# Performance work log

Hardware: AMD Instinct MI355X
Metric: run time of the kernel (lower is better)

Reference implementation:

```python
import jax, jax.numpy as jnp
import numpy as np

PATCH_LEN = 16
PATCH_STRIDE = 8
DIM = 512
NUM_HEADS = 8
HEAD_DIM = DIM // NUM_HEADS
NUM_LAYERS = 4
MLP_HIDDEN = 4 * DIM
ROPE_BASE = 10000.0
LN_EPS = 1e-5


def setup_inputs() -> dict:
    key = jax.random.key(0)
    ks = jax.random.split(key, 20)
    B, T, C = 4, 8192, 7
    s = 0.02
    inp = {
        "x": jax.random.normal(ks[0], (B, T, C), dtype=jnp.float32),
        "W_emb": jax.random.normal(ks[1], (PATCH_LEN * C, DIM), dtype=jnp.float32) * s,
        "b_emb": jnp.zeros((DIM,), jnp.float32),
        "ln1_g": jnp.ones((NUM_LAYERS, DIM), jnp.float32),
        "ln1_b": jnp.zeros((NUM_LAYERS, DIM), jnp.float32),
        "W_qkv": jax.random.normal(ks[2], (NUM_LAYERS, DIM, 3 * DIM), dtype=jnp.float32) * s,
        "b_qkv": jnp.zeros((NUM_LAYERS, 3 * DIM), jnp.float32),
        "W_proj": jax.random.normal(ks[3], (NUM_LAYERS, DIM, DIM), dtype=jnp.float32) * s,
        "b_proj": jnp.zeros((NUM_LAYERS, DIM), jnp.float32),
        "ln2_g": jnp.ones((NUM_LAYERS, DIM), jnp.float32),
        "ln2_b": jnp.zeros((NUM_LAYERS, DIM), jnp.float32),
        "W_mlp1": jax.random.normal(ks[4], (NUM_LAYERS, DIM, MLP_HIDDEN), dtype=jnp.float32) * s,
        "b_mlp1": jnp.zeros((NUM_LAYERS, MLP_HIDDEN), jnp.float32),
        "W_mlp2": jax.random.normal(ks[5], (NUM_LAYERS, MLP_HIDDEN, DIM), dtype=jnp.float32) * s,
        "b_mlp2": jnp.zeros((NUM_LAYERS, DIM), jnp.float32),
        "lnf_g": jnp.ones((DIM,), jnp.float32),
        "lnf_b": jnp.zeros((DIM,), jnp.float32),
    }
    return inp


def _layer_norm(x, g, b):
    mu = jnp.mean(x, axis=-1, keepdims=True)
    var = jnp.mean(jnp.square(x - mu), axis=-1, keepdims=True)
    return (x - mu) * jax.lax.rsqrt(var + LN_EPS) * g + b


def _rotate_half(x):
    x1, x2 = jnp.split(x, 2, axis=-1)
    return jnp.concatenate((-x2, x1), axis=-1)


def _rope_cos_sin(seq_len):
    t = jnp.arange(seq_len, dtype=jnp.float32)
    inv_freq = 1.0 / (ROPE_BASE ** (jnp.arange(0, HEAD_DIM, 2, dtype=jnp.float32) / HEAD_DIM))
    freqs = jnp.outer(t, inv_freq)                      # [L, hd/2]
    emb = jnp.concatenate((freqs, freqs), axis=-1)      # [L, hd]
    return jnp.cos(emb), jnp.sin(emb)


def _forward(x, W_emb, b_emb, ln1_g, ln1_b, W_qkv, b_qkv, W_proj, b_proj,
             ln2_g, ln2_b, W_mlp1, b_mlp1, W_mlp2, b_mlp2, lnf_g, lnf_b):
    B, T, C = x.shape
    n = (T - PATCH_LEN) // PATCH_STRIDE + 1
    # torch unfold: [B, n, C, patch_len], then flattened as (C, patch_len)
    idx = jnp.arange(n)[:, None] * PATCH_STRIDE + jnp.arange(PATCH_LEN)[None, :]  # [n, P]
    patches = x[:, idx, :]                              # [B, n, P, C]
    patches = patches.transpose(0, 1, 3, 2).reshape(B, n, C * PATCH_LEN)
    emb = patches @ W_emb + b_emb                       # [B, n, D]

    cos, sin = _rope_cos_sin(n)                         # [n, hd]
    cos = cos[None, None, :, :]
    sin = sin[None, None, :, :]
    scale = HEAD_DIM ** -0.5

    h = emb
    for i in range(NUM_LAYERS):
        # --- attention ---
        y = _layer_norm(h, ln1_g[i], ln1_b[i])
        qkv = (y @ W_qkv[i] + b_qkv[i]).reshape(B, n, 3, NUM_HEADS, HEAD_DIM)
        qkv = qkv.transpose(2, 0, 3, 1, 4)              # [3, B, H, n, hd]
        q, k, v = qkv[0], qkv[1], qkv[2]
        q = q * cos + _rotate_half(q) * sin
        k = k * cos + _rotate_half(k) * sin
        attn = jax.nn.softmax(jnp.einsum('bhqd,bhkd->bhqk', q, k) * scale, axis=-1)
        o = jnp.einsum('bhqk,bhkd->bhqd', attn, v)      # [B, H, n, hd]
        o = o.transpose(0, 2, 1, 3).reshape(B, n, DIM)
        h = h + (o @ W_proj[i] + b_proj[i])
        # --- mlp ---
        y = _layer_norm(h, ln2_g[i], ln2_b[i])
        y = jax.nn.gelu(y @ W_mlp1[i] + b_mlp1[i], approximate=False)
        h = h + (y @ W_mlp2[i] + b_mlp2[i])

    x_out = _layer_norm(h, lnf_g, lnf_b)
    return emb, x_out


def reference(x, W_emb, b_emb, ln1_g, ln1_b, W_qkv, b_qkv, W_proj, b_proj,
              ln2_g, ln2_b, W_mlp1, b_mlp1, W_mlp2, b_mlp2, lnf_g, lnf_b):
    return _forward(x, W_emb, b_emb, ln1_g, ln1_b, W_qkv, b_qkv, W_proj, b_proj,
                    ln2_g, ln2_b, W_mlp1, b_mlp1, W_mlp2, b_mlp2, lnf_g, lnf_b)
```

## Files before the change

### kernel.cpp

```cpp
#include <hip/hip_runtime.h>
#include <hip/hip_bf16.h>
#include <math.h>

#define B_SZ 4
#define T_LEN 8192
#define C_IN 7
#define NPATCH 1023
#define DIM 512
#define NH 8
#define HD 64
#define NLAYERS 4
#define MLP_HID 2048
#define M_ROWS (B_SZ * NPATCH)
#define KEMB 128
#define LN_EPS 1e-5f

typedef __attribute__((ext_vector_type(8))) short short8;
typedef __attribute__((ext_vector_type(4))) float float4v;

static __device__ __forceinline__ unsigned short f2bf(float f) {
  __hip_bfloat16 h = __float2bfloat16(f);
  return *reinterpret_cast<unsigned short*>(&h);
}
static __device__ __forceinline__ float bf2f(unsigned short u) {
  return __uint_as_float(((unsigned)u) << 16);
}

__global__ __launch_bounds__(256) void patch_kernel(
    const float* __restrict__ x, unsigned short* __restrict__ Pm) {
  int idx = blockIdx.x * 256 + threadIdx.x;
  if (idx >= M_ROWS * KEMB) return;
  int row = idx >> 7, c = idx & 127;
  float v = 0.f;
  if (c < 112) {
    int b = row / NPATCH, i = row - b * NPATCH;
    int ci = c >> 4, p = c & 15;
    v = x[((size_t)b * T_LEN + (size_t)i * 8 + p) * C_IN + ci];
  }
  Pm[idx] = f2bf(v);
}

__global__ __launch_bounds__(256) void wemb_cvt_kernel(
    const float* __restrict__ W, unsigned short* __restrict__ Wt) {
  int idx = blockIdx.x * 256 + threadIdx.x;
  if (idx >= DIM * KEMB) return;
  int n = idx >> 7, k = idx & 127;
  float v = (k < 112) ? W[(size_t)k * DIM + n] : 0.f;
  Wt[idx] = f2bf(v);
}

template <bool BF>
__global__ __launch_bounds__(256) void ln_kernel(
    const float* __restrict__ in, const float* __restrict__ g,
    const float* __restrict__ bb, void* __restrict__ outv, int M) {
  int row = blockIdx.x * 4 + (threadIdx.x >> 6);
  if (row >= M) return;
  int lane = threadIdx.x & 63;
  const float* xr = in + (size_t)row * DIM;
  float v[8];
  float s = 0.f;
  #pragma unroll
  for (int k = 0; k < 8; ++k) { v[k] = xr[lane + 64 * k]; s += v[k]; }
  #pragma unroll
  for (int off = 32; off; off >>= 1) s += __shfl_down(s, off);
  s = __shfl(s, 0);
  float mu = s * (1.f / DIM);
  float q = 0.f;
  #pragma unroll
  for (int k = 0; k < 8; ++k) { float d = v[k] - mu; q = fmaf(d, d, q); }
  #pragma unroll
  for (int off = 32; off; off >>= 1) q += __shfl_down(q, off);
  q = __shfl(q, 0);
  float rstd = rsqrtf(q * (1.f / DIM) + LN_EPS);
  #pragma unroll
  for (int k = 0; k < 8; ++k) {
    int d = lane + 64 * k;
    float r = (v[k] - mu) * rstd * g[d] + bb[d];
    if (BF)
      ((unsigned short*)outv)[(size_t)row * DIM + d] = f2bf(r);
    else
      ((float*)outv)[(size_t)row * DIM + d] = r;
  }
}

__global__ __launch_bounds__(256) void wcvt_kernel(
    const float* __restrict__ W, unsigned short* __restrict__ Wt, int K, int N) {
  __shared__ float tile[32][33];
  int n0 = blockIdx.x * 32, k0 = blockIdx.y * 32, L = blockIdx.z;
  const float* Ws = W + (size_t)L * K * N;
  unsigned short* Wd = Wt + (size_t)L * K * N;
  int tx = threadIdx.x & 31, ty = threadIdx.x >> 5;
  #pragma unroll
  for (int i = 0; i < 4; ++i)
    tile[ty + i * 8][tx] = Ws[(size_t)(k0 + ty + i * 8) * N + n0 + tx];
  __syncthreads();
  #pragma unroll
  for (int i = 0; i < 4; ++i)
    Wd[(size_t)(n0 + ty + i * 8) * K + k0 + tx] = f2bf(tile[tx][ty + i * 8]);
}

__global__ __launch_bounds__(256) void rope_tab_kernel(float2* __restrict__ tab) {
  int idx = blockIdx.x * 256 + threadIdx.x;
  if (idx >= NPATCH * 32) return;
  int i = idx >> 5, j = idx & 31;
  float inv = powf(10000.0f, -(float)j * (1.0f / 32.0f));
  float sn, cs;
  sincosf((float)i * inv, &sn, &cs);
  tab[idx] = make_float2(cs, sn);
}

template <int TM, int TN, int EPI>
__global__ __launch_bounds__(256) void mfma_gemm(
    const unsigned short* __restrict__ A, const unsigned short* __restrict__ Bt,
    const float* __restrict__ bias, const float* __restrict__ res,
    float* __restrict__ Cf, float* __restrict__ Cf2,
    unsigned short* __restrict__ Cb, const float2* __restrict__ rtab,
    int M, int N, int K) {
  constexpr int WM = TM / 2, WN = TN / 2;
  constexpr int NI = WM / 16, NJ = WN / 16;
  constexpr int ACH = TM * 4;
  constexpr int TCH = (TM + TN) * 4;
  constexpr int CH = TCH / 256;
  __shared__ __align__(16) unsigned short As[2][TM][40];
  __shared__ __align__(16) unsigned short Bs[2][TN][40];
  const int bm = blockIdx.y * TM;
  const int bn = blockIdx.x * TN;
  const int tid = threadIdx.x;
  const int lane = tid & 63, wave = tid >> 6;
  const int quad = lane >> 4, l16 = lane & 15;
  const int wm = (wave & 1) * WM;
  const int wn = (wave >> 1) * WN;

  float4v acc[NI][NJ];
  #pragma unroll
  for (int i = 0; i < NI; ++i)
    #pragma unroll
    for (int j = 0; j < NJ; ++j)
      acc[i][j] = (float4v){0.f, 0.f, 0.f, 0.f};

  uint4 pr[CH];
  auto load_regs = [&](int kk) {
    #pragma unroll
    for (int it = 0; it < CH; ++it) {
      int c = tid + it * 256;
      if (c < ACH) {
        int row = c >> 2, ch = (c & 3) * 8;
        int gm = bm + row;
        pr[it] = make_uint4(0u, 0u, 0u, 0u);
        if (gm < M) pr[it] = *(const uint4*)(A + (size_t)gm * K + kk + ch);
      } else {
        int c2 = c - ACH;
        int row = c2 >> 2, ch = (c2 & 3) * 8;
        pr[it] = *(const uint4*)(Bt + (size_t)(bn + row) * K + kk + ch);
      }
    }
  };

  load_regs(0);
  int buf = 0;
  for (int k0 = 0; k0 < K; k0 += 32, buf ^= 1) {
    #pragma unroll
    for (int it = 0; it < CH; ++it) {
      int c = tid + it * 256;
      if (c < ACH)
        *(uint4*)&As[buf][c >> 2][(c & 3) * 8] = pr[it];
      else {
        int c2 = c - ACH;
        *(uint4*)&Bs[buf][c2 >> 2][(c2 & 3) * 8] = pr[it];
      }
    }
    if (k0 + 32 < K) load_regs(k0 + 32);
    __syncthreads();
    short8 af[NI], bfr[NJ];
    #pragma unroll
    for (int i = 0; i < NI; ++i)
      af[i] = *(const short8*)&As[buf][wm + i * 16 + l16][quad * 8];
    #pragma unroll
    for (int j = 0; j < NJ; ++j)
      bfr[j] = *(const short8*)&Bs[buf][wn + j * 16 + l16][quad * 8];
    #pragma unroll
    for (int i = 0; i < NI; ++i)
      #pragma unroll
      for (int j = 0; j < NJ; ++j)
        acc[i][j] = __builtin_amdgcn_mfma_f32_16x16x32_bf16(
            af[i], bfr[j], acc[i][j], 0, 0, 0);
  }

  if (EPI == 6) {
    const int sec = (bn + wn) >> 9;
    #pragma unroll
    for (int i = 0; i < NI; ++i) {
      int gm0 = bm + wm + i * 16 + quad * 4;
      #pragma unroll
      for (int r = 0; r < 4; ++r) {
        int gm = gm0 + r;
        if (gm >= M) continue;
        size_t rowoff = (size_t)gm * N;
        if (sec < 2) {
          int ip = gm; if (ip >= 2046) ip -= 2046; if (ip >= 1023) ip -= 1023;
          float sc = (sec == 0) ? 0.125f : 1.f;
          #pragma unroll
          for (int j = 0; j < 2; ++j) {
            int gn = bn + wn + j * 16 + l16;
            float v0 = acc[i][j][r] + bias[gn];
            float v1 = acc[i][j + 2][r] + bias[gn + 32];
            float2 t = rtab[ip * 32 + j * 16 + l16];
            Cb[rowoff + gn]      = f2bf((v0 * t.x - v1 * t.y) * sc);
            Cb[rowoff + gn + 32] = f2bf((v1 * t.x + v0 * t.y) * sc);
          }
        } else {
          #pragma unroll
          for (int j = 0; j < 4; ++j) {
            int gn = bn + wn + j * 16 + l16;
            Cb[rowoff + gn] = f2bf(acc[i][j][r] + bias[gn]);
          }
        }
      }
    }
    return;
  }

  #pragma unroll
  for (int j = 0; j < NJ; ++j) {
    int gn = bn + wn + j * 16 + l16;
    float bv = bias[gn];
    #pragma unroll
    for (int i = 0; i < NI; ++i) {
      int gm0 = bm + wm + i * 16 + quad * 4;
      #pragma unroll
      for (int r = 0; r < 4; ++r) {
        int gm = gm0 + r;
        if (gm < M) {
          float v = acc[i][j][r] + bv;
          size_t off = (size_t)gm * N + gn;
          if (EPI == 1) {
            Cf[off] = v + res[off];
          } else if (EPI == 2) {
            Cb[off] = f2bf(0.5f * v * (1.f + erff(v * 0.70710678118f)));
          } else if (EPI == 3) {
            Cb[off] = f2bf(v);
          } else {
            Cf[off] = v;
            Cf2[off] = v;
          }
        }
      }
    }
  }
}

#define APITCH 72

__global__ __launch_bounds__(256) void attn_kernel(
    const unsigned short* __restrict__ qkvb, unsigned short* __restrict__ o) {
  const int qt0 = blockIdx.x * 64;
  const int h = blockIdx.y;
  const int b = blockIdx.z;
  const int tid = threadIdx.x;
  const int lane = tid & 63, wave = tid >> 6;
  const int quad = lane >> 4, l16 = lane & 15;

  __shared__ __align__(16) unsigned short Qs[64][APITCH];
  __shared__ __align__(16) unsigned short Ks[64][APITCH];
  __shared__ __align__(16) unsigned short Vt[HD][APITCH];
  __shared__ __align__(16) unsigned short Ps[4][16][APITCH];

  const int sr = tid >> 2;
  const int sc0 = (tid & 3) * 16;

  {
    int qi = qt0 + sr;
    uint4 a = make_uint4(0u, 0u, 0u, 0u), b2 = a;
    if (qi < NPATCH) {
      const uint4* src = (const uint4*)(qkvb + (size_t)(b * NPATCH + qi) * (3 * DIM) + h * HD + sc0);
      a = src[0]; b2 = src[1];
    }
    *(uint4*)&Qs[sr][sc0] = a;
    *(uint4*)&Qs[sr][sc0 + 8] = b2;
  }

  uint4 pk0, pk1, pv0, pv1;
  auto load_kv = [&](int j0) {
    int j = j0 + sr;
    pk0 = pk1 = pv0 = pv1 = make_uint4(0u, 0u, 0u, 0u);
    if (j < NPATCH) {
      const unsigned short* baseb = qkvb + (size_t)(b * NPATCH + j) * (3 * DIM) + h * HD;
      pk0 = *(const uint4*)(baseb + DIM + sc0);
      pk1 = *(const uint4*)(baseb + DIM + sc0 + 8);
      pv0 = *(const uint4*)(baseb + 2 * DIM + sc0);
      pv1 = *(const uint4*)(baseb + 2 * DIM + sc0 + 8);
    }
  };
  load_kv(0);
  __syncthreads();

  short8 aq0 = *(const short8*)&Qs[wave * 16 + l16][quad * 8];
  short8 aq1 = *(const short8*)&Qs[wave * 16 + l16][32 + quad * 8];

  float4v accO[4];
  #pragma unroll
  for (int j2 = 0; j2 < 4; ++j2) accO[j2] = (float4v){0.f, 0.f, 0.f, 0.f};
  float m_run[4] = {-1e30f, -1e30f, -1e30f, -1e30f};
  float l_run[4] = {0.f, 0.f, 0.f, 0.f};

  for (int j0 = 0; j0 < NPATCH; j0 += 64) {
    {
      *(uint4*)&Ks[sr][sc0] = pk0;
      *(uint4*)&Ks[sr][sc0 + 8] = pk1;
      unsigned short vs[16];
      *(uint4*)&vs[0] = pv0;
      *(uint4*)&vs[8] = pv1;
      #pragma unroll
      for (int u = 0; u < 16; ++u) Vt[sc0 + u][sr] = vs[u];
    }
    __syncthreads();
    if (j0 + 64 < NPATCH) load_kv(j0 + 64);

    float4v s[4];
    #pragma unroll
    for (int j = 0; j < 4; ++j) {
      s[j] = (float4v){0.f, 0.f, 0.f, 0.f};
      short8 bk0 = *(const short8*)&Ks[j * 16 + l16][quad * 8];
      short8 bk1 = *(const short8*)&Ks[j * 16 + l16][32 + quad * 8];
      s[j] = __builtin_amdgcn_mfma_f32_16x16x32_bf16(aq0, bk0, s[j], 0, 0, 0);
      s[j] = __builtin_amdgcn_mfma_f32_16x16x32_bf16(aq1, bk1, s[j], 0, 0, 0);
    }

    float mx[4], al[4], ts[4];
    #pragma unroll
    for (int r = 0; r < 4; ++r)
      mx[r] = fmaxf(fmaxf(s[0][r], s[1][r]), fmaxf(s[2][r], s[3][r]));
    #pragma unroll
    for (int mask = 1; mask < 16; mask <<= 1)
      #pragma unroll
      for (int r = 0; r < 4; ++r)
        mx[r] = fmaxf(mx[r], __shfl_xor(mx[r], mask));
    #pragma unroll
    for (int r = 0; r < 4; ++r) {
      float mnew = fmaxf(m_run[r], mx[r]);
      al[r] = __expf(m_run[r] - mnew);
      m_run[r] = mnew;
      ts[r] = 0.f;
    }
    #pragma unroll
    for (int j = 0; j < 4; ++j) {
      bool valid = (j0 + j * 16 + l16) < NPATCH;
      #pragma unroll
      for (int r = 0; r < 4; ++r) {
        float p = valid ? __expf(s[j][r] - m_run[r]) : 0.f;
        ts[r] += p;
        Ps[wave][quad * 4 + r][j * 16 + l16] = f2bf(p);
      }
    }
    #pragma unroll
    for (int mask = 1; mask < 16; mask <<= 1)
      #pragma unroll
      for (int r = 0; r < 4; ++r)
        ts[r] += __shfl_xor(ts[r], mask);
    #pragma unroll
    for (int r = 0; r < 4; ++r) l_run[r] = l_run[r] * al[r] + ts[r];
    #pragma unroll
    for (int j2 = 0; j2 < 4; ++j2)
      #pragma unroll
      for (int r = 0; r < 4; ++r)
        accO[j2][r] *= al[r];

    short8 pa0 = *(const short8*)&Ps[wave][l16][quad * 8];
    short8 pa1 = *(const short8*)&Ps[wave][l16][32 + quad * 8];
    #pragma unroll
    for (int j2 = 0; j2 < 4; ++j2) {
      short8 v0 = *(const short8*)&Vt[j2 * 16 + l16][quad * 8];
      short8 v1 = *(const short8*)&Vt[j2 * 16 + l16][32 + quad * 8];
      accO[j2] = __builtin_amdgcn_mfma_f32_16x16x32_bf16(pa0, v0, accO[j2], 0, 0, 0);
      accO[j2] = __builtin_amdgcn_mfma_f32_16x16x32_bf16(pa1, v1, accO[j2], 0, 0, 0);
    }
    __syncthreads();
  }

  #pragma unroll
  for (int r = 0; r < 4; ++r) {
    int qi = qt0 + wave * 16 + quad * 4 + r;
    if (qi < NPATCH) {
      float inv = 1.f / l_run[r];
      size_t off = (size_t)(b * NPATCH + qi) * DIM + h * HD + l16;
      #pragma unroll
      for (int j2 = 0; j2 < 4; ++j2)
        o[off + j2 * 16] = f2bf(accO[j2][r] * inv);
    }
  }
}

extern "C" void kernel_launch(void* const* d_in, const int* in_sizes, int n_in,
                              void* d_out, int out_size, void* d_ws, size_t ws_size,
                              hipStream_t stream) {
  const float* x      = (const float*)d_in[0];
  const float* W_emb  = (const float*)d_in[1];
  const float* b_emb  = (const float*)d_in[2];
  const float* ln1_g  = (const float*)d_in[3];
  const float* ln1_b  = (const float*)d_in[4];
  const float* W_qkv  = (const float*)d_in[5];
  const float* b_qkv  = (const float*)d_in[6];
  const float* W_proj = (const float*)d_in[7];
  const float* b_proj = (const float*)d_in[8];
  const float* ln2_g  = (const float*)d_in[9];
  const float* ln2_b  = (const float*)d_in[10];
  const float* W_mlp1 = (const float*)d_in[11];
  const float* b_mlp1 = (const float*)d_in[12];
  const float* W_mlp2 = (const float*)d_in[13];
  const float* b_mlp2 = (const float*)d_in[14];
  const float* lnf_g  = (const float*)d_in[15];
  const float* lnf_b  = (const float*)d_in[16];
  float* out = (float*)d_out;

  float* h              = (float*)d_ws;
  unsigned short* qkvb  = (unsigned short*)(h + (size_t)M_ROWS * DIM);
  unsigned short* midbf = qkvb;
  unsigned short* ybf   = qkvb + (size_t)M_ROWS * MLP_HID;
  unsigned short* obf   = ybf;
  unsigned short* wqkv_t  = ybf + (size_t)M_ROWS * DIM;
  unsigned short* wproj_t = wqkv_t  + (size_t)NLAYERS * DIM * 3 * DIM;
  unsigned short* wmlp1_t = wproj_t + (size_t)NLAYERS * DIM * DIM;
  unsigned short* wmlp2_t = wmlp1_t + (size_t)NLAYERS * DIM * MLP_HID;
  float2* rtab = (float2*)(wmlp2_t + (size_t)NLAYERS * MLP_HID * DIM);
  unsigned short* Pm    = (unsigned short*)(rtab + (size_t)NPATCH * 32);
  unsigned short* Wembt = Pm + (size_t)M_ROWS * KEMB;

  wcvt_kernel<<<dim3(3 * DIM / 32, DIM / 32, NLAYERS), 256, 0, stream>>>(W_qkv,  wqkv_t,  DIM, 3 * DIM);
  wcvt_kernel<<<dim3(DIM / 32, DIM / 32, NLAYERS),     256, 0, stream>>>(W_proj, wproj_t, DIM, DIM);
  wcvt_kernel<<<dim3(MLP_HID / 32, DIM / 32, NLAYERS), 256, 0, stream>>>(W_mlp1, wmlp1_t, DIM, MLP_HID);
  wcvt_kernel<<<dim3(DIM / 32, MLP_HID / 32, NLAYERS), 256, 0, stream>>>(W_mlp2, wmlp2_t, MLP_HID, DIM);
  rope_tab_kernel<<<(NPATCH * 32 + 255) / 256, 256, 0, stream>>>(rtab);
  patch_kernel<<<(M_ROWS * KEMB + 255) / 256, 256, 0, stream>>>(x, Pm);
  wemb_cvt_kernel<<<(DIM * KEMB + 255) / 256, 256, 0, stream>>>(W_emb, Wembt);

  const int MT64 = (M_ROWS + 63) / 64;
  const int LNG = (M_ROWS + 3) / 4;

  mfma_gemm<64, 64, 5><<<dim3(DIM / 64, MT64), 256, 0, stream>>>(
      Pm, Wembt, b_emb, nullptr, out, h, nullptr, nullptr, M_ROWS, DIM, KEMB);

  for (int L = 0; L < NLAYERS; ++L) {
    ln_kernel<true><<<LNG, 256, 0, stream>>>(h, ln1_g + L * DIM, ln1_b + L * DIM, ybf, M_ROWS);
    mfma_gemm<64, 128, 6><<<dim3(3 * DIM / 128, MT64), 256, 0, stream>>>(
        ybf, wqkv_t + (size_t)L * DIM * 3 * DIM, b_qkv + L * 3 * DIM,
        nullptr, nullptr, nullptr, qkvb, rtab, M_ROWS, 3 * DIM, DIM);
    attn_kernel<<<dim3((NPATCH + 63) / 64, NH, B_SZ), 256, 0, stream>>>(qkvb, obf);
    mfma_gemm<64, 64, 1><<<dim3(DIM / 64, MT64), 256, 0, stream>>>(
        obf, wproj_t + (size_t)L * DIM * DIM, b_proj + L * DIM,
        h, h, nullptr, nullptr, nullptr, M_ROWS, DIM, DIM);
    ln_kernel<true><<<LNG, 256, 0, stream>>>(h, ln2_g + L * DIM, ln2_b + L * DIM, ybf, M_ROWS);
    mfma_gemm<64, 128, 2><<<dim3(MLP_HID / 128, MT64), 256, 0, stream>>>(
        ybf, wmlp1_t + (size_t)L * DIM * MLP_HID, b_mlp1 + L * MLP_HID,
        nullptr, nullptr, nullptr, midbf, nullptr, M_ROWS, MLP_HID, DIM);
    mfma_gemm<64, 64, 1><<<dim3(DIM / 64, MT64), 256, 0, stream>>>(
        midbf, wmlp2_t + (size_t)L * MLP_HID * DIM, b_mlp2 + L * DIM,
        h, h, nullptr, nullptr, nullptr, M_ROWS, DIM, MLP_HID);
  }

  ln_kernel<false><<<LNG, 256, 0, stream>>>(h, lnf_g, lnf_b, out + (size_t)M_ROWS * DIM, M_ROWS);
}
```

Baseline: 694.2 us.

## Restructure attention loop: K in registers, double-buffered V, lazy rescale

The attention kernel now loads K tiles straight from global memory into registers in MFMA operand layout, which removes the K shared-memory tile. V is transposed into a double-buffered shared tile using packed 32-bit writes, so the trailing barrier per iteration goes away. The online softmax skips rescaling unless some row's max grows by more than a threshold, and the row-sum reduction is deferred to the end. MFMA sections are wrapped in s_setprio. In exchange it uses more registers for the K prefetch, and the lazy rescale relies on exponent headroom staying bounded.

```diff
diff --git a/kernel.cpp b/kernel.cpp
--- a/kernel.cpp
+++ b/kernel.cpp
@@ -261,13 +261,11 @@
   const int quad = lane >> 4, l16 = lane & 15;
 
   __shared__ __align__(16) unsigned short Qs[64][APITCH];
-  __shared__ __align__(16) unsigned short Ks[64][APITCH];
-  __shared__ __align__(16) unsigned short Vt[HD][APITCH];
+  __shared__ __align__(16) unsigned short Vt[2][HD][APITCH];
   __shared__ __align__(16) unsigned short Ps[4][16][APITCH];
 
   const int sr = tid >> 2;
   const int sc0 = (tid & 3) * 16;
-
   {
     int qi = qt0 + sr;
     uint4 a = make_uint4(0u, 0u, 0u, 0u), b2 = a;
@@ -279,19 +277,34 @@
     *(uint4*)&Qs[sr][sc0 + 8] = b2;
   }
 
-  uint4 pk0, pk1, pv0, pv1;
-  auto load_kv = [&](int j0) {
-    int j = j0 + sr;
-    pk0 = pk1 = pv0 = pv1 = make_uint4(0u, 0u, 0u, 0u);
-    if (j < NPATCH) {
-      const unsigned short* baseb = qkvb + (size_t)(b * NPATCH + j) * (3 * DIM) + h * HD;
-      pk0 = *(const uint4*)(baseb + DIM + sc0);
-      pk1 = *(const uint4*)(baseb + DIM + sc0 + 8);
-      pv0 = *(const uint4*)(baseb + 2 * DIM + sc0);
-      pv1 = *(const uint4*)(baseb + 2 * DIM + sc0 + 8);
-    }
+  const int kp = tid & 31, dg = tid >> 5;
+  uint4 pv0, pv1;
+  auto load_v = [&](int j0) {
+    pv0 = pv1 = make_uint4(0u, 0u, 0u, 0u);
+    int j = j0 + 2 * kp;
+    const unsigned short* vb = qkvb + (size_t)(b * NPATCH + j) * (3 * DIM) + 2 * DIM + h * HD + dg * 8;
+    if (j < NPATCH)     pv0 = *(const uint4*)vb;
+    if (j + 1 < NPATCH) pv1 = *(const uint4*)(vb + 3 * DIM);
   };
-  load_kv(0);
+
+  const unsigned short* kbase = qkvb + (size_t)b * NPATCH * (3 * DIM) + DIM + (size_t)h * HD;
+  uint4 nk0[4], nk1[4];
+  auto load_k = [&](int j0) {
+    #pragma unroll
+    for (int j = 0; j < 4; ++j) {
+      int row = j0 + j * 16 + l16;
+      nk0[j] = make_uint4(0u, 0u, 0u, 0u);
+      nk1[j] = nk0[j];
+      if (row < NPATCH) {
+        const uint4* kr = (const uint4*)(kbase + (size_t)row * (3 * DIM) + quad * 8);
+        nk0[j] = kr[0];
+        nk1[j] = kr[4];
+      }
+    }
+  };
+
+  load_v(0);
+  load_k(0);
   __syncthreads();
 
   short8 aq0 = *(const short8*)&Qs[wave * 16 + l16][quad * 8];
@@ -301,32 +314,37 @@
   #pragma unroll
   for (int j2 = 0; j2 < 4; ++j2) accO[j2] = (float4v){0.f, 0.f, 0.f, 0.f};
   float m_run[4] = {-1e30f, -1e30f, -1e30f, -1e30f};
-  float l_run[4] = {0.f, 0.f, 0.f, 0.f};
-
-  for (int j0 = 0; j0 < NPATCH; j0 += 64) {
+  float lp[4] = {0.f, 0.f, 0.f, 0.f};
+
+  int buf = 0;
+  for (int j0 = 0; j0 < NPATCH; j0 += 64, buf ^= 1) {
     {
-      *(uint4*)&Ks[sr][sc0] = pk0;
-      *(uint4*)&Ks[sr][sc0 + 8] = pk1;
-      unsigned short vs[16];
-      *(uint4*)&vs[0] = pv0;
-      *(uint4*)&vs[8] = pv1;
-      #pragma unroll
-      for (int u = 0; u < 16; ++u) Vt[sc0 + u][sr] = vs[u];
+      unsigned short va[8], vb8[8];
+      *(uint4*)&va[0] = pv0;
+      *(uint4*)&vb8[0] = pv1;
+      #pragma unroll
+      for (int u = 0; u < 8; ++u) {
+        unsigned pk = (unsigned)va[u] | ((unsigned)vb8[u] << 16);
+        *(unsigned*)&Vt[buf][dg * 8 + u][2 * kp] = pk;
+      }
     }
     __syncthreads();
-    if (j0 + 64 < NPATCH) load_kv(j0 + 64);
 
     float4v s[4];
+    __builtin_amdgcn_s_setprio(1);
     #pragma unroll
     for (int j = 0; j < 4; ++j) {
       s[j] = (float4v){0.f, 0.f, 0.f, 0.f};
-      short8 bk0 = *(const short8*)&Ks[j * 16 + l16][quad * 8];
-      short8 bk1 = *(const short8*)&Ks[j * 16 + l16][32 + quad * 8];
-      s[j] = __builtin_amdgcn_mfma_f32_16x16x32_bf16(aq0, bk0, s[j], 0, 0, 0);
-      s[j] = __builtin_amdgcn_mfma_f32_16x16x32_bf16(aq1, bk1, s[j], 0, 0, 0);
-    }
-
-    float mx[4], al[4], ts[4];
+      s[j] = __builtin_amdgcn_mfma_f32_16x16x32_bf16(
+          aq0, __builtin_bit_cast(short8, nk0[j]), s[j], 0, 0, 0);
+      s[j] = __builtin_amdgcn_mfma_f32_16x16x32_bf16(
+          aq1, __builtin_bit_cast(short8, nk1[j]), s[j], 0, 0, 0);
+    }
+    __builtin_amdgcn_s_setprio(0);
+
+    if (j0 + 64 < NPATCH) { load_k(j0 + 64); load_v(j0 + 64); }
+
+    float mx[4];
     #pragma unroll
     for (int r = 0; r < 4; ++r)
       mx[r] = fmaxf(fmaxf(s[0][r], s[1][r]), fmaxf(s[2][r], s[3][r]));
@@ -335,12 +353,18 @@
       #pragma unroll
       for (int r = 0; r < 4; ++r)
         mx[r] = fmaxf(mx[r], __shfl_xor(mx[r], mask));
-    #pragma unroll
-    for (int r = 0; r < 4; ++r) {
-      float mnew = fmaxf(m_run[r], mx[r]);
-      al[r] = __expf(m_run[r] - mnew);
-      m_run[r] = mnew;
-      ts[r] = 0.f;
+    float g = fmaxf(fmaxf(mx[0] - m_run[0], mx[1] - m_run[1]),
+                    fmaxf(mx[2] - m_run[2], mx[3] - m_run[3]));
+    if (!__all(g <= 8.f)) {
+      #pragma unroll
+      for (int r = 0; r < 4; ++r) {
+        float mnew = fmaxf(m_run[r], mx[r]);
+        float al = __expf(m_run[r] - mnew);
+        m_run[r] = mnew;
+        lp[r] *= al;
+        #pragma unroll
+        for (int j2 = 0; j2 < 4; ++j2) accO[j2][r] *= al;
+      }
     }
     #pragma unroll
     for (int j = 0; j < 4; ++j) {
@@ -348,40 +372,35 @@
       #pragma unroll
       for (int r = 0; r < 4; ++r) {
         float p = valid ? __expf(s[j][r] - m_run[r]) : 0.f;
-        ts[r] += p;
+        lp[r] += p;
         Ps[wave][quad * 4 + r][j * 16 + l16] = f2bf(p);
       }
     }
-    #pragma unroll
-    for (int mask = 1; mask < 16; mask <<= 1)
-      #pragma unroll
-      for (int r = 0; r < 4; ++r)
-        ts[r] += __shfl_xor(ts[r], mask);
-    #pragma unroll
-    for (int r = 0; r < 4; ++r) l_run[r] = l_run[r] * al[r] + ts[r];
-    #pragma unroll
-    for (int j2 = 0; j2 < 4; ++j2)
-      #pragma unroll
-      for (int r = 0; r < 4; ++r)
-        accO[j2][r] *= al[r];
 
     short8 pa0 = *(const short8*)&Ps[wave][l16][quad * 8];
     short8 pa1 = *(const short8*)&Ps[wave][l16][32 + quad * 8];
+    __builtin_amdgcn_s_setprio(1);
     #pragma unroll
     for (int j2 = 0; j2 < 4; ++j2) {
-      short8 v0 = *(const short8*)&Vt[j2 * 16 + l16][quad * 8];
-      short8 v1 = *(const short8*)&Vt[j2 * 16 + l16][32 + quad * 8];
+      short8 v0 = *(const short8*)&Vt[buf][j2 * 16 + l16][quad * 8];
+      short8 v1 = *(const short8*)&Vt[buf][j2 * 16 + l16][32 + quad * 8];
       accO[j2] = __builtin_amdgcn_mfma_f32_16x16x32_bf16(pa0, v0, accO[j2], 0, 0, 0);
       accO[j2] = __builtin_amdgcn_mfma_f32_16x16x32_bf16(pa1, v1, accO[j2], 0, 0, 0);
     }
-    __syncthreads();
-  }
+    __builtin_amdgcn_s_setprio(0);
+  }
+
+  #pragma unroll
+  for (int mask = 1; mask < 16; mask <<= 1)
+    #pragma unroll
+    for (int r = 0; r < 4; ++r)
+      lp[r] += __shfl_xor(lp[r], mask);
 
   #pragma unroll
   for (int r = 0; r < 4; ++r) {
     int qi = qt0 + wave * 16 + quad * 4 + r;
     if (qi < NPATCH) {
-      float inv = 1.f / l_run[r];
+      float inv = 1.f / lp[r];
       size_t off = (size_t)(b * NPATCH + qi) * DIM + h * HD + l16;
       #pragma unroll
       for (int j2 = 0; j2 < 4; ++j2)
```

Measured after the change: 712.4 us. 1.03x slower.
